# Kernel tuning notes

Measured on AMD Instinct MI355X. Metric: run time of the kernel, lower is better.

The kernel has to match this reference:

```python
import jax, jax.numpy as jnp
import numpy as np

V_SZ = 32000  # vocab_tar_size
D = 256       # embed / lstm / attn units
B, T, S = 32, 64, 128

def setup_inputs() -> dict:
    key = jax.random.key(0)
    ks = jax.random.split(key, 16)
    sc = lambda *shape: 1.0 / np.sqrt(shape[0])
    inp = {
        "tokens": jax.random.randint(ks[0], (B, T), 0, V_SZ),
        "h0": jax.random.normal(ks[1], (B, D), jnp.float32),
        "c0": jax.random.normal(ks[2], (B, D), jnp.float32),
        "enc_out": jax.random.normal(ks[3], (B, S, D), jnp.float32),
        # embedding table
        "E": jax.random.normal(ks[4], (V_SZ, D), jnp.float32) * 0.02,
        # attention: W1 (query), W2 (values/keys), V (score)
        "Wq": jax.random.normal(ks[5], (D, D), jnp.float32) * sc(D),
        "bq": jnp.zeros((D,), jnp.float32),
        "Wk": jax.random.normal(ks[6], (D, D), jnp.float32) * sc(D),
        "bk": jnp.zeros((D,), jnp.float32),
        "Vw": jax.random.normal(ks[7], (D, 1), jnp.float32) * sc(D),
        "bv": jnp.zeros((1,), jnp.float32),
        # LSTM: input dim 2D (context||embed), gates i,f,g,o
        "Wx": jax.random.normal(ks[8], (2 * D, 4 * D), jnp.float32) * sc(2 * D),
        "Wh": jax.random.normal(ks[9], (D, 4 * D), jnp.float32) * sc(D),
        "b_lstm": jnp.zeros((4 * D,), jnp.float32),
        # output projection + softmax
        "Wo": jax.random.normal(ks[10], (D, V_SZ), jnp.float32) * sc(D),
        "bo": jnp.zeros((V_SZ,), jnp.float32),
    }
    return inp


def reference(tokens, h0, c0, enc_out, E, Wq, bq, Wk, bk, Vw, bv,
              Wx, Wh, b_lstm, Wo, bo):
    # Precompute W2(values): same math as per-step recompute. [B,S,D]
    keys = enc_out @ Wk + bk

    def step(carry, tok):
        h, c = carry
        emb = E[tok]                                   # [B,D]
        # Bahdanau attention, query = h
        q = h @ Wq + bq                                # [B,D]
        score = jnp.tanh(q[:, None, :] + keys) @ Vw + bv   # [B,S,1]
        attn = jax.nn.softmax(score, axis=1)           # softmax over S
        ctx = jnp.sum(attn * enc_out, axis=1)          # [B,D]
        x = jnp.concatenate([ctx, emb], axis=-1)       # [B,2D]
        z = x @ Wx + h @ Wh + b_lstm                   # [B,4D]
        i, f, g, o = jnp.split(z, 4, axis=-1)          # keras gate order i,f,c,o
        c_new = jax.nn.sigmoid(f) * c + jax.nn.sigmoid(i) * jnp.tanh(g)
        h_new = jax.nn.sigmoid(o) * jnp.tanh(c_new)
        probs = jax.nn.softmax(h_new @ Wo + bo, axis=-1)   # [B,V]
        return (h_new, c_new), probs

    (_, _), outs = jax.lax.scan(step, (h0, c0), tokens.T)  # outs: [T,B,V]
    return jnp.transpose(outs, (1, 0, 2))                  # [B,T,V]
```

## Files before the change

### kernel.cpp

```cpp
#include <hip/hip_runtime.h>

#define Bz 32
#define Tz 64
#define Sz 128
#define Dz 256
#define Vz 32000
#define NLG 250

__device__ __forceinline__ float sigmf(float x){ return 1.0f/(1.0f + __expf(-x)); }
__device__ __forceinline__ float tanhfast(float x){ float e = __expf(2.0f*x); return 1.0f - 2.0f/(e+1.0f); }

__device__ __forceinline__ void st_l3(float* p, float v){
  __hip_atomic_store(p, v, __ATOMIC_RELAXED, __HIP_MEMORY_SCOPE_AGENT);
}
__device__ __forceinline__ float ld_l3(const float* p){
  return __hip_atomic_load(p, __ATOMIC_RELAXED, __HIP_MEMORY_SCOPE_AGENT);
}

__global__ void __launch_bounds__(256) k_prep(const float* __restrict__ enc,
                                              const float* __restrict__ Wk,
                                              const float* __restrict__ bk,
                                              const float* __restrict__ Wx,
                                              const float* __restrict__ E,
                                              const int* __restrict__ tok,
                                              float* __restrict__ keys,
                                              float* __restrict__ encW,
                                              float* __restrict__ embW,
                                              unsigned* __restrict__ flags){
  const int blk = blockIdx.x, tid = threadIdx.x;
  if (blk == 0) flags[tid] = 0u;
  if (blk < 256){
    const int b  = blk >> 3;
    const int s0 = (blk & 7) * 16;
    const float* ebase = enc + (b*Sz + s0)*Dz;
    const int d = tid;
    float acc[16];
    #pragma unroll
    for (int i = 0; i < 16; ++i) acc[i] = 0.f;
    for (int k = 0; k < Dz; k += 4){
      float w0 = Wk[(k+0)*Dz + d], w1 = Wk[(k+1)*Dz + d];
      float w2 = Wk[(k+2)*Dz + d], w3 = Wk[(k+3)*Dz + d];
      #pragma unroll
      for (int si = 0; si < 16; ++si){
        float4 ev = *(const float4*)(ebase + si*Dz + k);
        acc[si] += ev.x*w0 + ev.y*w1 + ev.z*w2 + ev.w*w3;
      }
    }
    const float bkd = bk[d];
    #pragma unroll
    for (int si = 0; si < 16; ++si)
      keys[(b*Sz + s0 + si)*Dz + d] = acc[si] + bkd;
  } else if (blk < 1280){
    const int row0 = (blk - 256) * 4;
    const int u4 = tid * 4;
    float4 a0 = {0,0,0,0}, a1 = {0,0,0,0}, a2 = {0,0,0,0}, a3 = {0,0,0,0};
    for (int d = 0; d < Dz; ++d){
      float4 wv = *(const float4*)(Wx + (size_t)d*1024 + u4);
      float e0 = enc[(size_t)(row0+0)*Dz + d];
      float e1 = enc[(size_t)(row0+1)*Dz + d];
      float e2 = enc[(size_t)(row0+2)*Dz + d];
      float e3 = enc[(size_t)(row0+3)*Dz + d];
      a0.x += e0*wv.x; a0.y += e0*wv.y; a0.z += e0*wv.z; a0.w += e0*wv.w;
      a1.x += e1*wv.x; a1.y += e1*wv.y; a1.z += e1*wv.z; a1.w += e1*wv.w;
      a2.x += e2*wv.x; a2.y += e2*wv.y; a2.z += e2*wv.z; a2.w += e2*wv.w;
      a3.x += e3*wv.x; a3.y += e3*wv.y; a3.z += e3*wv.z; a3.w += e3*wv.w;
    }
    *(float4*)(encW + (size_t)(row0+0)*1024 + u4) = a0;
    *(float4*)(encW + (size_t)(row0+1)*1024 + u4) = a1;
    *(float4*)(encW + (size_t)(row0+2)*1024 + u4) = a2;
    *(float4*)(encW + (size_t)(row0+3)*1024 + u4) = a3;
  } else {
    const int bt0 = (blk - 1280) * 4;
    const int u4 = tid * 4;
    const float* e0p = E + (size_t)tok[bt0+0]*Dz;
    const float* e1p = E + (size_t)tok[bt0+1]*Dz;
    const float* e2p = E + (size_t)tok[bt0+2]*Dz;
    const float* e3p = E + (size_t)tok[bt0+3]*Dz;
    float4 a0 = {0,0,0,0}, a1 = {0,0,0,0}, a2 = {0,0,0,0}, a3 = {0,0,0,0};
    for (int d = 0; d < Dz; ++d){
      float4 wv = *(const float4*)(Wx + (size_t)(256 + d)*1024 + u4);
      float e0 = e0p[d], e1 = e1p[d], e2 = e2p[d], e3 = e3p[d];
      a0.x += e0*wv.x; a0.y += e0*wv.y; a0.z += e0*wv.z; a0.w += e0*wv.w;
      a1.x += e1*wv.x; a1.y += e1*wv.y; a1.z += e1*wv.z; a1.w += e1*wv.w;
      a2.x += e2*wv.x; a2.y += e2*wv.y; a2.z += e2*wv.z; a2.w += e2*wv.w;
      a3.x += e3*wv.x; a3.y += e3*wv.y; a3.z += e3*wv.z; a3.w += e3*wv.w;
    }
    *(float4*)(embW + (size_t)(bt0+0)*1024 + u4) = a0;
    *(float4*)(embW + (size_t)(bt0+1)*1024 + u4) = a1;
    *(float4*)(embW + (size_t)(bt0+2)*1024 + u4) = a2;
    *(float4*)(embW + (size_t)(bt0+3)*1024 + u4) = a3;
  }
}

__global__ void __launch_bounds__(1024) k_recur(
    const float* __restrict__ h0, const float* __restrict__ c0,
    const float* __restrict__ Wq, const float* __restrict__ bq,
    const float* __restrict__ Vw, const float* __restrict__ bv,
    const float* __restrict__ Wh, const float* __restrict__ bl,
    const float* __restrict__ keys, const float* __restrict__ encW,
    const float* __restrict__ embW,
    float* __restrict__ hs, float* xch, unsigned* flags)
{
  __shared__ float smem[27776];
  float* ew    = smem;
  float* wql   = ew + 16384;
  float* qv    = wql + 8192;
  float* hlds  = qv + 256;
  float* vl    = hlds + 256;
  float* selds = vl + 256;
  float* zpa   = selds + 128;
  float* zpb   = zpa + 1024;
  float* hnl   = zpb + 1024;
  float* clds  = hnl + 32;
  float* ebw   = clds + 32;
  float* bll   = ebw + 128;

  const int tid = threadIdx.x;
  const int blk = blockIdx.x;
  const int b = ((blk >> 6) << 3) | (blk & 7);
  const int s = (blk >> 3) & 7;
  const int lidx = b*8 + s;

  const int kc = tid >> 7, ul = tid & 127;
  const int u_gate = ((ul >> 5) << 8) + (s << 5) + (ul & 31);

  #pragma unroll
  for (int i = 0; i < 16; ++i){
    int idx = tid + i*1024;
    int srow = idx >> 7, uu = idx & 127;
    int ug = ((uu >> 5) << 8) + (s << 5) + (uu & 31);
    ew[idx] = encW[(size_t)(b*Sz + srow)*1024 + ug];
  }
  #pragma unroll
  for (int i = 0; i < 8; ++i){
    int idx = tid + i*1024;
    wql[idx] = Wq[(size_t)(s*32)*Dz + idx];
  }
  float w[32];
  #pragma unroll
  for (int i = 0; i < 32; ++i) w[i] = Wh[(size_t)(kc*32 + i)*1024 + u_gate];

  if (tid < Dz) vl[tid] = Vw[tid];
  if (tid >= 256 && tid < 384) bll[tid-256] = bl[((tid-256) >> 5)*Dz + s*32 + ((tid-256) & 31)];
  if (tid < 32){
    hnl[tid]  = h0[b*Dz + s*32 + tid];
    clds[tid] = c0[b*Dz + s*32 + tid];
  }
  __syncthreads();

  {
    float* xn = xch + (size_t)lidx*288;
    if (tid < 256){
      float qp = 0.f;
      #pragma unroll
      for (int u = 0; u < 32; ++u) qp = __builtin_fmaf(hnl[u], wql[u*256 + tid], qp);
      st_l3(xn + tid, qp);
    } else if (tid < 288){
      st_l3(xn + tid, hnl[tid - 256]);
    }
    __syncthreads();
    if (tid == 0)
      __hip_atomic_store(flags + lidx, 1u, __ATOMIC_RELAXED, __HIP_MEMORY_SCOPE_AGENT);
  }

  const float bv0 = bv[0];
  const int ss = tid >> 3, p8 = tid & 7;

  for (int t = 0; t < Tz; ++t){
    if (tid < 8){
      const unsigned tgt = (unsigned)(t + 1);
      while (__hip_atomic_load(flags + b*8 + tid, __ATOMIC_RELAXED, __HIP_MEMORY_SCOPE_AGENT) < tgt)
        __builtin_amdgcn_s_sleep(1);
    }
    __syncthreads();
    __builtin_amdgcn_fence(__ATOMIC_ACQUIRE, "workgroup");

    const float* xcp = xch + (size_t)((t & 1)*256 + b*8)*288;
    if (tid < 256){
      float q = bq[tid];
      #pragma unroll
      for (int s2 = 0; s2 < 8; ++s2) q += ld_l3(xcp + s2*288 + tid);
      qv[tid] = q;
    } else if (tid >= 512 && tid < 768){
      const int hu = tid - 512;
      hlds[hu] = ld_l3(xcp + (hu >> 5)*288 + 256 + (hu & 31));
    } else if (tid >= 768 && tid < 896){
      const int i = tid - 768;
      ebw[i] = embW[((size_t)b*Tz + t)*1024 + (i >> 5)*Dz + s*32 + (i & 31)];
    }
    __syncthreads();
    {
      const float* kp = keys + (size_t)(b*Sz + ss)*Dz;
      float a = 0.f;
      #pragma unroll
      for (int j = 0; j < 8; ++j){
        const int d0 = j*32 + p8*4;
        float4 kv = *(const float4*)(kp + d0);
        float4 qj = *(const float4*)(qv + d0);
        float4 vj = *(const float4*)(vl + d0);
        a += tanhfast(qj.x + kv.x) * vj.x;
        a += tanhfast(qj.y + kv.y) * vj.y;
        a += tanhfast(qj.z + kv.z) * vj.z;
        a += tanhfast(qj.w + kv.w) * vj.w;
      }
      a += __shfl_down(a, 4);
      a += __shfl_down(a, 2);
      a += __shfl_down(a, 1);
      if (p8 == 0) selds[ss] = __expf(a + bv0);
    }
    __syncthreads();
    {
      float a1 = 0.f;
      const float* hp = hlds + kc*32;
      #pragma unroll
      for (int i = 0; i < 32; ++i) a1 = __builtin_fmaf(hp[i], w[i], a1);
      float a2 = 0.f;
      const float* ewp = ew + (kc*16)*128 + ul;
      #pragma unroll
      for (int m = 0; m < 16; ++m)
        a2 = __builtin_fmaf(selds[kc*16 + m], ewp[m*128], a2);
      zpa[kc*128 + ul] = a1;
      zpb[kc*128 + ul] = a2;
    }
    __syncthreads();
    if (tid < 32){
      float dsum = 0.f;
      #pragma unroll
      for (int m = 0; m < 32; ++m){
        float4 sv = *(const float4*)(selds + m*4);
        dsum += sv.x + sv.y + sv.z + sv.w;
      }
      const float inv = 1.0f / dsum;
      const int u = tid;
      float z[4];
      #pragma unroll
      for (int g = 0; g < 4; ++g){
        float za = 0.f, zb = 0.f;
        #pragma unroll
        for (int k2 = 0; k2 < 8; ++k2){
          za += zpa[k2*128 + g*32 + u];
          zb += zpb[k2*128 + g*32 + u];
        }
        z[g] = bll[g*32 + u] + ebw[g*32 + u] + za + inv*zb;
      }
      float cn = sigmf(z[1])*clds[u] + sigmf(z[0])*tanhfast(z[2]);
      float hn = sigmf(z[3])*tanhfast(cn);
      clds[u] = cn; hnl[u] = hn;
      hs[(size_t)(t*Bz + b)*Dz + s*32 + u] = hn;
    }
    __syncthreads();
    {
      float* xn = xch + (size_t)(((t+1) & 1)*256 + lidx)*288;
      if (tid < 256){
        float qp = 0.f;
        #pragma unroll
        for (int u = 0; u < 32; ++u) qp = __builtin_fmaf(hnl[u], wql[u*256 + tid], qp);
        st_l3(xn + tid, qp);
      } else if (tid < 288){
        st_l3(xn + tid, hnl[tid - 256]);
      }
      __syncthreads();
      if (tid == 0)
        __hip_atomic_store(flags + lidx, (unsigned)(t + 2), __ATOMIC_RELAXED, __HIP_MEMORY_SCOPE_AGENT);
    }
  }
}

__global__ void __launch_bounds__(1024) k_logits(
    const float* __restrict__ hs, const float* __restrict__ Wo, const float* __restrict__ bo,
    float* __restrict__ out, float* __restrict__ part)
{
  __shared__ float smem[38144];
  float* Bs     = smem;
  float* As     = Bs + 256*132;
  float* rs_row = As + 32*132;

  const int tid = threadIdx.x;
  const int wid = blockIdx.x;
  const int c0  = wid * 128;
  const int ty = tid >> 5, tx = tid & 31;

  #pragma unroll
  for (int i = 0; i < 8; ++i){
    int idx = tid + i*1024;
    int k = idx >> 5, c4 = idx & 31;
    *(float4*)(Bs + k*132 + c4*4) = *(const float4*)(Wo + (size_t)k*Vz + c0 + c4*4);
  }
  const float4 bo4 = *(const float4*)(bo + c0 + tx*4);
  __syncthreads();

  for (int y = 0; y < 16; ++y){
    const int R0 = y * 128;
    float acc[4][4];
    #pragma unroll
    for (int i = 0; i < 4; ++i)
      #pragma unroll
      for (int j = 0; j < 4; ++j) acc[i][j] = 0.f;

    for (int k0 = 0; k0 < Dz; k0 += 32){
      {
        int r = tid >> 3, kq = tid & 7;
        float4 hv = *(const float4*)(hs + (size_t)(R0 + r)*Dz + k0 + kq*4);
        As[(kq*4+0)*132 + r] = hv.x; As[(kq*4+1)*132 + r] = hv.y;
        As[(kq*4+2)*132 + r] = hv.z; As[(kq*4+3)*132 + r] = hv.w;
      }
      __syncthreads();
      #pragma unroll
      for (int kk = 0; kk < 32; ++kk){
        float4 av  = *(const float4*)(As + kk*132 + ty*4);
        float4 bb  = *(const float4*)(Bs + (k0+kk)*132 + tx*4);
        float ar[4] = {av.x, av.y, av.z, av.w};
        float br[4] = {bb.x, bb.y, bb.z, bb.w};
        #pragma unroll
        for (int i = 0; i < 4; ++i)
          #pragma unroll
          for (int j = 0; j < 4; ++j)
            acc[i][j] = __builtin_fmaf(ar[i], br[j], acc[i][j]);
      }
      __syncthreads();
    }
    #pragma unroll
    for (int i = 0; i < 4; ++i){
      const int R = R0 + ty*4 + i;
      const int orow = (R & 31)*64 + (R >> 5);
      float4 o;
      o.x = __expf(acc[i][0] + bo4.x);
      o.y = __expf(acc[i][1] + bo4.y);
      o.z = __expf(acc[i][2] + bo4.z);
      o.w = __expf(acc[i][3] + bo4.w);
      *(float4*)(out + (size_t)orow*Vz + c0 + tx*4) = o;
      float rp = o.x + o.y + o.z + o.w;
      #pragma unroll
      for (int off = 16; off > 0; off >>= 1) rp += __shfl_down(rp, off, 32);
      if (tx == 0) rs_row[ty*4 + i] = rp;
    }
    __syncthreads();
    if (tid < 128)
      part[(size_t)wid*2048 + R0 + tid] = rs_row[tid];
    __syncthreads();
  }
}

__global__ void __launch_bounds__(256) k_scale(float* __restrict__ out, const float* __restrict__ part){
  const int row = blockIdx.x;
  const int b = row >> 6, tt = row & 63;
  const int R = tt*Bz + b;
  const int tid = threadIdx.x;
  __shared__ float ssum[4];
  float v = (tid < NLG) ? part[(size_t)tid*2048 + R] : 0.f;
  #pragma unroll
  for (int off = 32; off > 0; off >>= 1) v += __shfl_down(v, off);
  if ((tid & 63) == 0) ssum[tid >> 6] = v;
  __syncthreads();
  const float inv = 1.0f / (ssum[0] + ssum[1] + ssum[2] + ssum[3]);
  float4* rp = (float4*)(out + (size_t)row*Vz);
  for (int j4 = tid; j4 < Vz/4; j4 += 256){
    float4 x = rp[j4];
    x.x *= inv; x.y *= inv; x.z *= inv; x.w *= inv;
    rp[j4] = x;
  }
}

extern "C" void kernel_launch(void* const* d_in, const int* in_sizes, int n_in,
                              void* d_out, int out_size, void* d_ws, size_t ws_size,
                              hipStream_t stream){
  const int*   tok = (const int*)  d_in[0];
  const float* h0  = (const float*)d_in[1];
  const float* c0  = (const float*)d_in[2];
  const float* enc = (const float*)d_in[3];
  const float* E   = (const float*)d_in[4];
  const float* Wq  = (const float*)d_in[5];
  const float* bq  = (const float*)d_in[6];
  const float* Wk  = (const float*)d_in[7];
  const float* bk  = (const float*)d_in[8];
  const float* Vw  = (const float*)d_in[9];
  const float* bv  = (const float*)d_in[10];
  const float* Wx  = (const float*)d_in[11];
  const float* Wh  = (const float*)d_in[12];
  const float* bl  = (const float*)d_in[13];
  const float* Wo  = (const float*)d_in[14];
  const float* bo  = (const float*)d_in[15];
  float* out = (float*)d_out;
  float* ws  = (float*)d_ws;

  float* keys = ws;
  float* encW = keys + 1048576;
  float* embW = encW + 4194304;
  float* hs   = embW + 2097152;
  float* xch  = hs   + 524288;
  float* part = xch  + 147456;
  unsigned* flags = (unsigned*)(part + 512000);

  hipLaunchKernelGGL(k_prep, dim3(1792), dim3(256), 0, stream,
                     enc, Wk, bk, Wx, E, tok, keys, encW, embW, flags);
  hipLaunchKernelGGL(k_recur, dim3(256), dim3(1024), 0, stream,
                     h0, c0, Wq, bq, Vw, bv, Wh, bl, keys, encW, embW,
                     hs, xch, flags);
  hipLaunchKernelGGL(k_logits, dim3(NLG), dim3(1024), 0, stream,
                     hs, Wo, bo, out, part);
  hipLaunchKernelGGL(k_scale, dim3(2048), dim3(256), 0, stream, out, part);
}
```

Before: 1.835 ms.

## Cut per-step block barriers in recurrent kernel by moving LSTM tail to one wave

```diff
diff --git a/kernel.cpp b/kernel.cpp
--- a/kernel.cpp
+++ b/kernel.cpp
@@ -101,25 +101,26 @@
     const float* __restrict__ embW,
     float* __restrict__ hs, float* xch, unsigned* flags)
 {
-  __shared__ float smem[27776];
+  __shared__ float smem[27960];
   float* ew    = smem;
   float* wql   = ew + 16384;
   float* qv    = wql + 8192;
   float* hlds  = qv + 256;
   float* vl    = hlds + 256;
   float* selds = vl + 256;
-  float* zpa   = selds + 128;
+  float* zpa   = selds + 132;
   float* zpb   = zpa + 1024;
   float* hnl   = zpb + 1024;
   float* clds  = hnl + 32;
   float* ebw   = clds + 32;
-  float* bll   = ebw + 128;
+  float* bll   = ebw + 256;
 
   const int tid = threadIdx.x;
   const int blk = blockIdx.x;
   const int b = ((blk >> 6) << 3) | (blk & 7);
   const int s = (blk >> 3) & 7;
   const int lidx = b*8 + s;
+  const int wave = tid >> 6, lane = tid & 63;
 
   const int kc = tid >> 7, ul = tid & 127;
   const int u_gate = ((ul >> 5) << 8) + (s << 5) + (ul & 31);
@@ -148,18 +149,25 @@
   }
   __syncthreads();
 
-  {
+  if (wave == 0){
     float* xn = xch + (size_t)lidx*288;
-    if (tid < 256){
-      float qp = 0.f;
-      #pragma unroll
-      for (int u = 0; u < 32; ++u) qp = __builtin_fmaf(hnl[u], wql[u*256 + tid], qp);
-      st_l3(xn + tid, qp);
-    } else if (tid < 288){
-      st_l3(xn + tid, hnl[tid - 256]);
-    }
-    __syncthreads();
-    if (tid == 0)
+    float4 qp = {0.f, 0.f, 0.f, 0.f};
+    #pragma unroll
+    for (int u = 0; u < 32; ++u){
+      float hu_ = hnl[u];
+      float4 wv = *(const float4*)(wql + u*256 + lane*4);
+      qp.x = __builtin_fmaf(hu_, wv.x, qp.x);
+      qp.y = __builtin_fmaf(hu_, wv.y, qp.y);
+      qp.z = __builtin_fmaf(hu_, wv.z, qp.z);
+      qp.w = __builtin_fmaf(hu_, wv.w, qp.w);
+    }
+    st_l3(xn + lane*4 + 0, qp.x);
+    st_l3(xn + lane*4 + 1, qp.y);
+    st_l3(xn + lane*4 + 2, qp.z);
+    st_l3(xn + lane*4 + 3, qp.w);
+    if (lane < 32) st_l3(xn + 256 + lane, hnl[lane]);
+    asm volatile("s_waitcnt vmcnt(0)" ::: "memory");
+    if (lane == 0)
       __hip_atomic_store(flags + lidx, 1u, __ATOMIC_RELAXED, __HIP_MEMORY_SCOPE_AGENT);
   }
 
@@ -167,28 +175,34 @@
   const int ss = tid >> 3, p8 = tid & 7;
 
   for (int t = 0; t < Tz; ++t){
-    if (tid < 8){
-      const unsigned tgt = (unsigned)(t + 1);
-      while (__hip_atomic_load(flags + b*8 + tid, __ATOMIC_RELAXED, __HIP_MEMORY_SCOPE_AGENT) < tgt)
-        __builtin_amdgcn_s_sleep(1);
+    if (wave >= 2 && wave <= 9){
+      if (lane < 8){
+        const unsigned tgt = (unsigned)(t + 1);
+        while (__hip_atomic_load(flags + b*8 + lane, __ATOMIC_RELAXED, __HIP_MEMORY_SCOPE_AGENT) < tgt)
+          __builtin_amdgcn_s_sleep(1);
+      }
+      __builtin_amdgcn_fence(__ATOMIC_ACQUIRE, "workgroup");
+      const float* xcp = xch + (size_t)((t & 1)*256 + b*8)*288;
+      if (wave < 6){
+        const int d = tid - 128;
+        float q = bq[d];
+        #pragma unroll
+        for (int s2 = 0; s2 < 8; ++s2) q += ld_l3(xcp + s2*288 + d);
+        qv[d] = q;
+      } else {
+        const int hu = tid - 384;
+        hlds[hu] = ld_l3(xcp + (hu >> 5)*288 + 256 + (hu & 31));
+      }
+    } else if (wave == 1){
+      const float* ep = embW + ((size_t)b*Tz + t)*1024;
+      #pragma unroll
+      for (int rr = 0; rr < 2; ++rr){
+        int i = lane + rr*64;
+        ebw[(t & 1)*128 + i] = ep[(i >> 5)*Dz + s*32 + (i & 31)];
+      }
     }
     __syncthreads();
-    __builtin_amdgcn_fence(__ATOMIC_ACQUIRE, "workgroup");
-
-    const float* xcp = xch + (size_t)((t & 1)*256 + b*8)*288;
-    if (tid < 256){
-      float q = bq[tid];
-      #pragma unroll
-      for (int s2 = 0; s2 < 8; ++s2) q += ld_l3(xcp + s2*288 + tid);
-      qv[tid] = q;
-    } else if (tid >= 512 && tid < 768){
-      const int hu = tid - 512;
-      hlds[hu] = ld_l3(xcp + (hu >> 5)*288 + 256 + (hu & 31));
-    } else if (tid >= 768 && tid < 896){
-      const int i = tid - 768;
-      ebw[i] = embW[((size_t)b*Tz + t)*1024 + (i >> 5)*Dz + s*32 + (i & 31)];
-    }
-    __syncthreads();
+
     {
       const float* kp = keys + (size_t)(b*Sz + ss)*Dz;
       float a = 0.f;
@@ -207,60 +221,70 @@
       a += __shfl_down(a, 2);
       a += __shfl_down(a, 1);
       if (p8 == 0) selds[ss] = __expf(a + bv0);
-    }
-    __syncthreads();
-    {
+
       float a1 = 0.f;
       const float* hp = hlds + kc*32;
       #pragma unroll
       for (int i = 0; i < 32; ++i) a1 = __builtin_fmaf(hp[i], w[i], a1);
+      zpa[kc*128 + ul] = a1;
+    }
+    __syncthreads();
+
+    {
       float a2 = 0.f;
       const float* ewp = ew + (kc*16)*128 + ul;
       #pragma unroll
       for (int m = 0; m < 16; ++m)
         a2 = __builtin_fmaf(selds[kc*16 + m], ewp[m*128], a2);
-      zpa[kc*128 + ul] = a1;
       zpb[kc*128 + ul] = a2;
+      if (wave == 15){
+        const int l = lane;
+        float v = selds[l] + selds[l + 64];
+        #pragma unroll
+        for (int off = 32; off > 0; off >>= 1) v += __shfl_down(v, off);
+        if (l == 0) selds[Sz] = 1.0f / v;
+      }
     }
     __syncthreads();
-    if (tid < 32){
-      float dsum = 0.f;
-      #pragma unroll
-      for (int m = 0; m < 32; ++m){
-        float4 sv = *(const float4*)(selds + m*4);
-        dsum += sv.x + sv.y + sv.z + sv.w;
-      }
-      const float inv = 1.0f / dsum;
-      const int u = tid;
-      float z[4];
-      #pragma unroll
-      for (int g = 0; g < 4; ++g){
-        float za = 0.f, zb = 0.f;
+
+    if (wave == 0){
+      if (lane < 32){
+        const int u = lane;
+        const float inv = selds[Sz];
+        float z[4];
         #pragma unroll
-        for (int k2 = 0; k2 < 8; ++k2){
-          za += zpa[k2*128 + g*32 + u];
-          zb += zpb[k2*128 + g*32 + u];
+        for (int g = 0; g < 4; ++g){
+          float za = 0.f, zb = 0.f;
+          #pragma unroll
+          for (int k2 = 0; k2 < 8; ++k2){
+            za += zpa[k2*128 + g*32 + u];
+            zb += zpb[k2*128 + g*32 + u];
+          }
+          z[g] = bll[g*32 + u] + ebw[(t & 1)*128 + g*32 + u] + za + inv*zb;
         }
-        z[g] = bll[g*32 + u] + ebw[g*32 + u] + za + inv*zb;
-      }
-      float cn = sigmf(z[1])*clds[u] + sigmf(z[0])*tanhfast(z[2]);
-      float hn = sigmf(z[3])*tanhfast(cn);
-      clds[u] = cn; hnl[u] = hn;
-      hs[(size_t)(t*Bz + b)*Dz + s*32 + u] = hn;
-    }
-    __syncthreads();
-    {
+        float cn = sigmf(z[1])*clds[u] + sigmf(z[0])*tanhfast(z[2]);
+        float hn = sigmf(z[3])*tanhfast(cn);
+        clds[u] = cn; hnl[u] = hn;
+        hs[(size_t)(t*Bz + b)*Dz + s*32 + u] = hn;
+      }
       float* xn = xch + (size_t)(((t+1) & 1)*256 + lidx)*288;
-      if (tid < 256){
-        float qp = 0.f;
-        #pragma unroll
-        for (int u = 0; u < 32; ++u) qp = __builtin_fmaf(hnl[u], wql[u*256 + tid], qp);
-        st_l3(xn + tid, qp);
-      } else if (tid < 288){
-        st_l3(xn + tid, hnl[tid - 256]);
-      }
-      __syncthreads();
-      if (tid == 0)
+      float4 qp = {0.f, 0.f, 0.f, 0.f};
+      #pragma unroll
+      for (int u = 0; u < 32; ++u){
+        float hu_ = hnl[u];
+        float4 wv = *(const float4*)(wql + u*256 + lane*4);
+        qp.x = __builtin_fmaf(hu_, wv.x, qp.x);
+        qp.y = __builtin_fmaf(hu_, wv.y, qp.y);
+        qp.z = __builtin_fmaf(hu_, wv.z, qp.z);
+        qp.w = __builtin_fmaf(hu_, wv.w, qp.w);
+      }
+      st_l3(xn + lane*4 + 0, qp.x);
+      st_l3(xn + lane*4 + 1, qp.y);
+      st_l3(xn + lane*4 + 2, qp.z);
+      st_l3(xn + lane*4 + 3, qp.w);
+      if (lane < 32) st_l3(xn + 256 + lane, hnl[lane]);
+      asm volatile("s_waitcnt vmcnt(0)" ::: "memory");
+      if (lane == 0)
         __hip_atomic_store(flags + lidx, (unsigned)(t + 2), __ATOMIC_RELAXED, __HIP_MEMORY_SCOPE_AGENT);
     }
   }
```

Measured after the change: 1.653 ms. 9.9% less time.
